# Kernel tuning notes

Hardware: AMD Instinct MI355X
Metric: run time of the kernel (lower is better)

Reference implementation:

```python
import jax, jax.numpy as jnp
import numpy as np

THRESH = 1.0
SLOPE = 25.0  # fast_sigmoid surrogate slope
B, T, C_IN = 64, 512, 32
HID, TS, K = 128, 4, 3
C_OUT = HID * TS

@jax.custom_vjp
def spike_fn(x):
    # Heaviside forward, fast-sigmoid surrogate backward (matches snntorch surrogate.fast_sigmoid(slope=25))
    return (x > 0).astype(x.dtype)

def _spike_fwd(x):
    return spike_fn(x), x

def _spike_bwd(x, g):
    return (g / (SLOPE * jnp.abs(x) + 1.0) ** 2,)

spike_fn.defvjp(_spike_fwd, _spike_bwd)


def setup_inputs() -> dict:
    key = jax.random.key(0)
    ks = jax.random.split(key, 4)
    return {
        "x": jax.random.normal(ks[0], (B, T, C_IN), jnp.float32),
        "conv_w": jax.random.normal(ks[1], (C_OUT, C_IN, K), jnp.float32) / np.sqrt(C_IN * K).astype(np.float32),
        "conv_b": jax.random.normal(ks[2], (C_OUT,), jnp.float32) * 0.01,
        "bn_gamma": jnp.ones((C_OUT,), jnp.float32),
        "bn_beta": jnp.zeros((C_OUT,), jnp.float32),
        "bn_mean": jax.random.normal(ks[3], (C_OUT,), jnp.float32) * 0.1,
        "bn_var": jnp.ones((C_OUT,), jnp.float32),
        "lif_beta": jnp.full((HID,), 0.9, jnp.float32),
    }


def reference(x, conv_w, conv_b, bn_gamma, bn_beta, bn_mean, bn_var, lif_beta):
    # Conv1d(input -> hidden*Ts, k=3, pad=1): x (B,T,C) -> NCH layout
    h = jax.lax.conv_general_dilated(
        x.transpose(0, 2, 1), conv_w, (1,), [(K // 2, K // 2)],
        dimension_numbers=("NCH", "OIH", "NCH"))  # (B, C_OUT, T)
    h = h + conv_b[None, :, None]
    # BatchNorm1d in eval mode (running stats)
    scale = bn_gamma * jax.lax.rsqrt(bn_var + 1e-5)
    h = (h - bn_mean[None, :, None]) * scale[None, :, None] + bn_beta[None, :, None]
    # (B, C_OUT, T) -> (B, T, Ts, HID) -> (Ts*T, B, HID) time-major spike input
    h = h.transpose(0, 2, 1).reshape(B, T * TS, HID).transpose(1, 0, 2)

    beta = jnp.clip(lif_beta, 0.0, 1.0)

    def step(mem, h_t):
        # snntorch Leaky (reset_mechanism='subtract'): reset from previous mem, detached
        reset = jax.lax.stop_gradient((mem > THRESH).astype(mem.dtype))
        mem = beta * mem + h_t - reset * THRESH
        spk = spike_fn(mem - THRESH)
        return mem, (spk, mem)

    mem0 = jnp.zeros((B, HID), x.dtype)
    _, (spk_rec, mem_rec) = jax.lax.scan(step, mem0, h)
    return spk_rec, mem_rec  # each (Ts*T, B, HID)
```

## Files before the change

kernel.cpp:

```cpp
#include <hip/hip_runtime.h>

#define T_LEN 512
#define CIN   32
#define HIDN  128
#define TSUB  4
#define NB    64
#define TT    64
#define NT2   2048
#define COLS  8192
#define CHUNK 32
#define NCHUNK (NT2 / CHUNK)

#define HT_IDX(s, col, t) ((((size_t)(s) * COLS + (size_t)(col)) * T_LEN) + (size_t)(t))

__global__ __launch_bounds__(256) void conv_bn_kernel(
    const float* __restrict__ x,
    const float* __restrict__ w,
    const float* __restrict__ cb,
    const float* __restrict__ gam,
    const float* __restrict__ bet,
    const float* __restrict__ mean,
    const float* __restrict__ var,
    float* __restrict__ hT)
{
    __shared__ float xs[66 * 36];
    __shared__ float ws[128 * 100];
    __shared__ float scs[128];
    __shared__ float bbs[128];

    const int t0  = blockIdx.x * TT;
    const int s   = blockIdx.y;
    const int b   = blockIdx.z;
    const int tid = threadIdx.x;

    for (int idx = tid; idx < 66 * 32; idx += 256) {
        int r = idx >> 5, ci = idx & 31;
        int t = t0 + r - 1;
        xs[r * 36 + ci] = (t >= 0 && t < T_LEN) ? x[(b * T_LEN + t) * CIN + ci] : 0.0f;
    }
    for (int idx = tid; idx < 128 * 96; idx += 256) {
        int row = idx / 96, j = idx - row * 96;
        int k = j >> 5, i = j & 31;
        ws[row * 100 + j] = w[(s * HIDN + row) * (CIN * 3) + i * 3 + k];
    }
    if (tid < 128) {
        int c = s * HIDN + tid;
        float sc = gam[c] * rsqrtf(var[c] + 1e-5f);
        scs[tid] = sc;
        bbs[tid] = (cb[c] - mean[c]) * sc + bet[c];
    }
    __syncthreads();

    const int tc = tid & 31;
    const int tt = tid >> 5;

    float acc[4][8];
#pragma unroll
    for (int a = 0; a < 4; ++a)
#pragma unroll
        for (int q = 0; q < 8; ++q) acc[a][q] = 0.0f;

    for (int j0 = 0; j0 < 96; j0 += 4) {
        const int k  = j0 >> 5;
        const int i0 = j0 & 31;
        float4 wv[4];
#pragma unroll
        for (int cc = 0; cc < 4; ++cc)
            wv[cc] = *reinterpret_cast<const float4*>(&ws[(tc + cc * 32) * 100 + j0]);
#pragma unroll
        for (int tq = 0; tq < 8; ++tq) {
            float4 xv = *reinterpret_cast<const float4*>(&xs[(tt * 8 + tq + k) * 36 + i0]);
#pragma unroll
            for (int cc = 0; cc < 4; ++cc) {
                acc[cc][tq] = fmaf(wv[cc].x, xv.x, acc[cc][tq]);
                acc[cc][tq] = fmaf(wv[cc].y, xv.y, acc[cc][tq]);
                acc[cc][tq] = fmaf(wv[cc].z, xv.z, acc[cc][tq]);
                acc[cc][tq] = fmaf(wv[cc].w, xv.w, acc[cc][tq]);
            }
        }
    }

#pragma unroll
    for (int cc = 0; cc < 4; ++cc) {
        const int hid = tc + cc * 32;
        const float sc = scs[hid], bb = bbs[hid];
        float4 v0, v1;
        v0.x = fmaf(acc[cc][0], sc, bb);
        v0.y = fmaf(acc[cc][1], sc, bb);
        v0.z = fmaf(acc[cc][2], sc, bb);
        v0.w = fmaf(acc[cc][3], sc, bb);
        v1.x = fmaf(acc[cc][4], sc, bb);
        v1.y = fmaf(acc[cc][5], sc, bb);
        v1.z = fmaf(acc[cc][6], sc, bb);
        v1.w = fmaf(acc[cc][7], sc, bb);
        float* dst = hT + HT_IDX(s, b * HIDN + hid, t0 + tt * 8);
        *reinterpret_cast<float4*>(dst)     = v0;
        *reinterpret_cast<float4*>(dst + 4) = v1;
    }
}

__global__ __launch_bounds__(64) void lif_pass1_kernel(
    const float* __restrict__ hT,
    const float* __restrict__ lifb,
    float* __restrict__ out)
{
    const int col = blockIdx.x * 64 + threadIdx.x;
    const int hid = col & (HIDN - 1);
    float beta = fminf(fmaxf(lifb[hid], 0.0f), 1.0f);

    float* __restrict__ memo = out + (size_t)NT2 * COLS;

    const float4* p[4];
#pragma unroll
    for (int s = 0; s < 4; ++s)
        p[s] = reinterpret_cast<const float4*>(hT + HT_IDX(s, col, 0));

    float4 hq[4][4];
#pragma unroll
    for (int bq = 0; bq < 4; ++bq)
#pragma unroll
        for (int s = 0; s < 4; ++s) hq[bq][s] = p[s][bq];

    float mem = 0.0f;

    for (int m0 = 0; m0 < 128; m0 += 4) {
#pragma unroll
        for (int bq = 0; bq < 4; ++bq) {
            const int m = m0 + bq;
            const float* hb = reinterpret_cast<const float*>(&hq[bq][0]);
#pragma unroll
            for (int j = 0; j < 16; ++j) {
                const float hval = hb[(j & 3) * 4 + (j >> 2)];
                const float reset = (mem > 1.0f) ? 1.0f : 0.0f;
                mem = __fsub_rn(__fadd_rn(__fmul_rn(beta, mem), hval), reset);
                if (j == 15 && (bq & 1) == 1) {
                    const int tp = m * 16 + 15;
                    if (tp < NT2 - 1)
                        memo[(size_t)tp * COLS + col] = mem;
                }
            }
            if (m + 4 < 128) {
#pragma unroll
                for (int s = 0; s < 4; ++s) hq[bq][s] = p[s][m + 4];
            }
        }
    }
}

__global__ __launch_bounds__(256) void lif_pass2_kernel(
    const float* __restrict__ hT,
    const float* __restrict__ lifb,
    float* __restrict__ out)
{
    const int chunk = blockIdx.y;
    const int col   = blockIdx.x * 256 + threadIdx.x;
    const int hid   = col & (HIDN - 1);
    float beta = fminf(fmaxf(lifb[hid], 0.0f), 1.0f);

    float* __restrict__ spk  = out;
    float* __restrict__ memo = out + (size_t)NT2 * COLS;

    const int tpb = chunk * CHUNK;
    const int tb  = tpb >> 2;

    float4 hq[4][2];
#pragma unroll
    for (int s = 0; s < 4; ++s) {
        const float4* ps = reinterpret_cast<const float4*>(hT + HT_IDX(s, col, tb));
        hq[s][0] = ps[0];
        hq[s][1] = ps[1];
    }

    float mem = (chunk == 0) ? 0.0f : memo[(size_t)(tpb - 1) * COLS + col];

#pragma unroll
    for (int j = 0; j < 32; ++j) {
        const float* hb = reinterpret_cast<const float*>(&hq[j & 3][0]);
        const float hval = hb[j >> 2];
        const float reset = (mem > 1.0f) ? 1.0f : 0.0f;
        mem = __fsub_rn(__fadd_rn(__fmul_rn(beta, mem), hval), reset);
        const size_t idx = (size_t)(tpb + j) * COLS + col;
        spk[idx]  = (mem > 1.0f) ? 1.0f : 0.0f;
        memo[idx] = mem;
    }
}

extern "C" void kernel_launch(void* const* d_in, const int* in_sizes, int n_in,
                              void* d_out, int out_size, void* d_ws, size_t ws_size,
                              hipStream_t stream) {
    const float* x    = (const float*)d_in[0];
    const float* w    = (const float*)d_in[1];
    const float* cb   = (const float*)d_in[2];
    const float* gam  = (const float*)d_in[3];
    const float* bet  = (const float*)d_in[4];
    const float* mean = (const float*)d_in[5];
    const float* var  = (const float*)d_in[6];
    const float* lifb = (const float*)d_in[7];

    float* hT = (float*)d_ws;

    dim3 gA(T_LEN / TT, TSUB, NB);
    conv_bn_kernel<<<gA, 256, 0, stream>>>(x, w, cb, gam, bet, mean, var, hT);

    lif_pass1_kernel<<<COLS / 64, 64, 0, stream>>>(hT, lifb, (float*)d_out);

    dim3 gC(COLS / 256, NCHUNK);
    lif_pass2_kernel<<<gC, 256, 0, stream>>>(hT, lifb, (float*)d_out);
}
```

Baseline: 268.3 us.

## Split conv channels per block, checkpoint every 16 steps, pair columns in LIF replay

The conv kernel now handles 64 channels per block instead of 128, doubling the grid and halving shared memory and accumulator registers to raise occupancy. Pass 1 now stores a membrane checkpoint every 16 steps instead of every 32, and its register buffers are flattened into named variables via macros. Pass 2 replays 16-step chunks with each thread handling two adjacent columns, writing float2 to spike and membrane outputs. This trades more checkpoint stores and more conv blocks for shorter serial replay chains and wider stores, though the 2-column layout leaves half as many threads per chunk.

```diff
diff --git a/kernel.cpp b/kernel.cpp
--- a/kernel.cpp
+++ b/kernel.cpp
@@ -8,8 +8,6 @@
 #define TT    64
 #define NT2   2048
 #define COLS  8192
-#define CHUNK 32
-#define NCHUNK (NT2 / CHUNK)
 
 #define HT_IDX(s, col, t) ((((size_t)(s) * COLS + (size_t)(col)) * T_LEN) + (size_t)(t))
 
@@ -24,12 +22,14 @@
     float* __restrict__ hT)
 {
     __shared__ float xs[66 * 36];
-    __shared__ float ws[128 * 100];
-    __shared__ float scs[128];
-    __shared__ float bbs[128];
+    __shared__ float ws[64 * 100];
+    __shared__ float scs[64];
+    __shared__ float bbs[64];
 
     const int t0  = blockIdx.x * TT;
-    const int s   = blockIdx.y;
+    const int sg  = blockIdx.y;
+    const int s   = sg >> 1;
+    const int ch0 = (sg & 1) * 64;
     const int b   = blockIdx.z;
     const int tid = threadIdx.x;
 
@@ -38,13 +38,13 @@
         int t = t0 + r - 1;
         xs[r * 36 + ci] = (t >= 0 && t < T_LEN) ? x[(b * T_LEN + t) * CIN + ci] : 0.0f;
     }
-    for (int idx = tid; idx < 128 * 96; idx += 256) {
+    for (int idx = tid; idx < 64 * 96; idx += 256) {
         int row = idx / 96, j = idx - row * 96;
         int k = j >> 5, i = j & 31;
-        ws[row * 100 + j] = w[(s * HIDN + row) * (CIN * 3) + i * 3 + k];
-    }
-    if (tid < 128) {
-        int c = s * HIDN + tid;
+        ws[row * 100 + j] = w[(s * HIDN + ch0 + row) * (CIN * 3) + i * 3 + k];
+    }
+    if (tid < 64) {
+        int c = s * HIDN + ch0 + tid;
         float sc = gam[c] * rsqrtf(var[c] + 1e-5f);
         scs[tid] = sc;
         bbs[tid] = (cb[c] - mean[c]) * sc + bet[c];
@@ -54,24 +54,24 @@
     const int tc = tid & 31;
     const int tt = tid >> 5;
 
-    float acc[4][8];
-#pragma unroll
-    for (int a = 0; a < 4; ++a)
+    float acc[2][8];
+#pragma unroll
+    for (int a = 0; a < 2; ++a)
 #pragma unroll
         for (int q = 0; q < 8; ++q) acc[a][q] = 0.0f;
 
     for (int j0 = 0; j0 < 96; j0 += 4) {
         const int k  = j0 >> 5;
         const int i0 = j0 & 31;
-        float4 wv[4];
-#pragma unroll
-        for (int cc = 0; cc < 4; ++cc)
+        float4 wv[2];
+#pragma unroll
+        for (int cc = 0; cc < 2; ++cc)
             wv[cc] = *reinterpret_cast<const float4*>(&ws[(tc + cc * 32) * 100 + j0]);
 #pragma unroll
         for (int tq = 0; tq < 8; ++tq) {
             float4 xv = *reinterpret_cast<const float4*>(&xs[(tt * 8 + tq + k) * 36 + i0]);
 #pragma unroll
-            for (int cc = 0; cc < 4; ++cc) {
+            for (int cc = 0; cc < 2; ++cc) {
                 acc[cc][tq] = fmaf(wv[cc].x, xv.x, acc[cc][tq]);
                 acc[cc][tq] = fmaf(wv[cc].y, xv.y, acc[cc][tq]);
                 acc[cc][tq] = fmaf(wv[cc].z, xv.z, acc[cc][tq]);
@@ -81,9 +81,9 @@
     }
 
 #pragma unroll
-    for (int cc = 0; cc < 4; ++cc) {
-        const int hid = tc + cc * 32;
-        const float sc = scs[hid], bb = bbs[hid];
+    for (int cc = 0; cc < 2; ++cc) {
+        const int cl = tc + cc * 32;
+        const float sc = scs[cl], bb = bbs[cl];
         float4 v0, v1;
         v0.x = fmaf(acc[cc][0], sc, bb);
         v0.y = fmaf(acc[cc][1], sc, bb);
@@ -93,11 +93,26 @@
         v1.y = fmaf(acc[cc][5], sc, bb);
         v1.z = fmaf(acc[cc][6], sc, bb);
         v1.w = fmaf(acc[cc][7], sc, bb);
-        float* dst = hT + HT_IDX(s, b * HIDN + hid, t0 + tt * 8);
+        float* dst = hT + HT_IDX(s, b * HIDN + ch0 + cl, t0 + tt * 8);
         *reinterpret_cast<float4*>(dst)     = v0;
         *reinterpret_cast<float4*>(dst + 4) = v1;
     }
 }
+
+#define LIF_STEP(HVAL) { \
+    const float reset = (mem > 1.0f) ? 1.0f : 0.0f; \
+    mem = __fsub_rn(__fadd_rn(__fmul_rn(beta, mem), (HVAL)), reset); }
+
+#define SLOT16(B) { \
+    LIF_STEP((hq##B##0).x) LIF_STEP((hq##B##1).x) LIF_STEP((hq##B##2).x) LIF_STEP((hq##B##3).x) \
+    LIF_STEP((hq##B##0).y) LIF_STEP((hq##B##1).y) LIF_STEP((hq##B##2).y) LIF_STEP((hq##B##3).y) \
+    LIF_STEP((hq##B##0).z) LIF_STEP((hq##B##1).z) LIF_STEP((hq##B##2).z) LIF_STEP((hq##B##3).z) \
+    LIF_STEP((hq##B##0).w) LIF_STEP((hq##B##1).w) LIF_STEP((hq##B##2).w) LIF_STEP((hq##B##3).w) \
+    { const int tp = (m0 + B) * 16 + 15; \
+      if (tp < NT2 - 1) memo[(size_t)tp * COLS + col] = mem; } \
+    if (m0 + B + 4 < 128) { \
+        hq##B##0 = p0[m0 + B + 4]; hq##B##1 = p1[m0 + B + 4]; \
+        hq##B##2 = p2[m0 + B + 4]; hq##B##3 = p3[m0 + B + 4]; } }
 
 __global__ __launch_bounds__(64) void lif_pass1_kernel(
     const float* __restrict__ hT,
@@ -110,42 +125,35 @@
 
     float* __restrict__ memo = out + (size_t)NT2 * COLS;
 
-    const float4* p[4];
-#pragma unroll
-    for (int s = 0; s < 4; ++s)
-        p[s] = reinterpret_cast<const float4*>(hT + HT_IDX(s, col, 0));
-
-    float4 hq[4][4];
-#pragma unroll
-    for (int bq = 0; bq < 4; ++bq)
-#pragma unroll
-        for (int s = 0; s < 4; ++s) hq[bq][s] = p[s][bq];
+    const float4* p0 = reinterpret_cast<const float4*>(hT + HT_IDX(0, col, 0));
+    const float4* p1 = reinterpret_cast<const float4*>(hT + HT_IDX(1, col, 0));
+    const float4* p2 = reinterpret_cast<const float4*>(hT + HT_IDX(2, col, 0));
+    const float4* p3 = reinterpret_cast<const float4*>(hT + HT_IDX(3, col, 0));
+
+    float4 hq00 = p0[0], hq01 = p1[0], hq02 = p2[0], hq03 = p3[0];
+    float4 hq10 = p0[1], hq11 = p1[1], hq12 = p2[1], hq13 = p3[1];
+    float4 hq20 = p0[2], hq21 = p1[2], hq22 = p2[2], hq23 = p3[2];
+    float4 hq30 = p0[3], hq31 = p1[3], hq32 = p2[3], hq33 = p3[3];
 
     float mem = 0.0f;
 
     for (int m0 = 0; m0 < 128; m0 += 4) {
-#pragma unroll
-        for (int bq = 0; bq < 4; ++bq) {
-            const int m = m0 + bq;
-            const float* hb = reinterpret_cast<const float*>(&hq[bq][0]);
-#pragma unroll
-            for (int j = 0; j < 16; ++j) {
-                const float hval = hb[(j & 3) * 4 + (j >> 2)];
-                const float reset = (mem > 1.0f) ? 1.0f : 0.0f;
-                mem = __fsub_rn(__fadd_rn(__fmul_rn(beta, mem), hval), reset);
-                if (j == 15 && (bq & 1) == 1) {
-                    const int tp = m * 16 + 15;
-                    if (tp < NT2 - 1)
-                        memo[(size_t)tp * COLS + col] = mem;
-                }
-            }
-            if (m + 4 < 128) {
-#pragma unroll
-                for (int s = 0; s < 4; ++s) hq[bq][s] = p[s][m + 4];
-            }
-        }
-    }
-}
+        SLOT16(0)
+        SLOT16(1)
+        SLOT16(2)
+        SLOT16(3)
+    }
+}
+
+#define P2_STEP(HV0, HV1, J) { \
+    const float r0 = (m0v > 1.0f) ? 1.0f : 0.0f; \
+    const float r1 = (m1v > 1.0f) ? 1.0f : 0.0f; \
+    m0v = __fsub_rn(__fadd_rn(__fmul_rn(b0, m0v), (HV0)), r0); \
+    m1v = __fsub_rn(__fadd_rn(__fmul_rn(b1, m1v), (HV1)), r1); \
+    const size_t o = (size_t)(tpb + (J)) * COLS + col0; \
+    *reinterpret_cast<float2*>(spk + o)  = \
+        make_float2((m0v > 1.0f) ? 1.0f : 0.0f, (m1v > 1.0f) ? 1.0f : 0.0f); \
+    *reinterpret_cast<float2*>(memo + o) = make_float2(m0v, m1v); }
 
 __global__ __launch_bounds__(256) void lif_pass2_kernel(
     const float* __restrict__ hT,
@@ -153,36 +161,38 @@
     float* __restrict__ out)
 {
     const int chunk = blockIdx.y;
-    const int col   = blockIdx.x * 256 + threadIdx.x;
-    const int hid   = col & (HIDN - 1);
-    float beta = fminf(fmaxf(lifb[hid], 0.0f), 1.0f);
+    const int c2    = blockIdx.x * 256 + threadIdx.x;
+    const int col0  = c2 * 2;
+    const float b0 = fminf(fmaxf(lifb[col0 & (HIDN - 1)], 0.0f), 1.0f);
+    const float b1 = fminf(fmaxf(lifb[(col0 + 1) & (HIDN - 1)], 0.0f), 1.0f);
 
     float* __restrict__ spk  = out;
     float* __restrict__ memo = out + (size_t)NT2 * COLS;
 
-    const int tpb = chunk * CHUNK;
+    const int tpb = chunk * 16;
     const int tb  = tpb >> 2;
 
-    float4 hq[4][2];
-#pragma unroll
-    for (int s = 0; s < 4; ++s) {
-        const float4* ps = reinterpret_cast<const float4*>(hT + HT_IDX(s, col, tb));
-        hq[s][0] = ps[0];
-        hq[s][1] = ps[1];
-    }
-
-    float mem = (chunk == 0) ? 0.0f : memo[(size_t)(tpb - 1) * COLS + col];
-
-#pragma unroll
-    for (int j = 0; j < 32; ++j) {
-        const float* hb = reinterpret_cast<const float*>(&hq[j & 3][0]);
-        const float hval = hb[j >> 2];
-        const float reset = (mem > 1.0f) ? 1.0f : 0.0f;
-        mem = __fsub_rn(__fadd_rn(__fmul_rn(beta, mem), hval), reset);
-        const size_t idx = (size_t)(tpb + j) * COLS + col;
-        spk[idx]  = (mem > 1.0f) ? 1.0f : 0.0f;
-        memo[idx] = mem;
-    }
+    const float4 a0 = *reinterpret_cast<const float4*>(hT + HT_IDX(0, col0, tb));
+    const float4 a1 = *reinterpret_cast<const float4*>(hT + HT_IDX(1, col0, tb));
+    const float4 a2 = *reinterpret_cast<const float4*>(hT + HT_IDX(2, col0, tb));
+    const float4 a3 = *reinterpret_cast<const float4*>(hT + HT_IDX(3, col0, tb));
+    const float4 c0 = *reinterpret_cast<const float4*>(hT + HT_IDX(0, col0 + 1, tb));
+    const float4 c1 = *reinterpret_cast<const float4*>(hT + HT_IDX(1, col0 + 1, tb));
+    const float4 c2v= *reinterpret_cast<const float4*>(hT + HT_IDX(2, col0 + 1, tb));
+    const float4 c3 = *reinterpret_cast<const float4*>(hT + HT_IDX(3, col0 + 1, tb));
+
+    float m0v = 0.0f, m1v = 0.0f;
+    if (chunk != 0) {
+        const float2 ck = *reinterpret_cast<const float2*>(
+            memo + (size_t)(tpb - 1) * COLS + col0);
+        m0v = ck.x;
+        m1v = ck.y;
+    }
+
+    P2_STEP(a0.x, c0.x,  0) P2_STEP(a1.x, c1.x,  1) P2_STEP(a2.x, c2v.x,  2) P2_STEP(a3.x, c3.x,  3)
+    P2_STEP(a0.y, c0.y,  4) P2_STEP(a1.y, c1.y,  5) P2_STEP(a2.y, c2v.y,  6) P2_STEP(a3.y, c3.y,  7)
+    P2_STEP(a0.z, c0.z,  8) P2_STEP(a1.z, c1.z,  9) P2_STEP(a2.z, c2v.z, 10) P2_STEP(a3.z, c3.z, 11)
+    P2_STEP(a0.w, c0.w, 12) P2_STEP(a1.w, c1.w, 13) P2_STEP(a2.w, c2v.w, 14) P2_STEP(a3.w, c3.w, 15)
 }
 
 extern "C" void kernel_launch(void* const* d_in, const int* in_sizes, int n_in,
@@ -199,11 +209,11 @@
 
     float* hT = (float*)d_ws;
 
-    dim3 gA(T_LEN / TT, TSUB, NB);
+    dim3 gA(T_LEN / TT, 8, NB);
     conv_bn_kernel<<<gA, 256, 0, stream>>>(x, w, cb, gam, bet, mean, var, hT);
 
     lif_pass1_kernel<<<COLS / 64, 64, 0, stream>>>(hT, lifb, (float*)d_out);
 
-    dim3 gC(COLS / 256, NCHUNK);
+    dim3 gC(COLS / 2 / 256, NT2 / 16);
     lif_pass2_kernel<<<gC, 256, 0, stream>>>(hT, lifb, (float*)d_out);
 }
```

Result: faster. 262.0 us (-2.4%).
